# Kernel tuning notes

Hardware: AMD Instinct MI355X
Metric: run time of the kernel (lower is better)

Reference implementation:

```python
import jax, jax.numpy as jnp
import numpy as np

FIELD_DIMS = [100000, 50000, 20000, 10000, 5000, 2000, 1000, 500, 100, 26]
ORDER = 3
EMBED_DIM = 64


def setup_inputs() -> dict:
    key = jax.random.key(0)
    k1, k2, k3 = jax.random.split(key, 3)
    total = sum(FIELD_DIMS)  # 188626
    num_fields = len(FIELD_DIMS)
    batch = 16384
    x = jax.random.randint(k1, (batch, num_fields), 0, 26, dtype=jnp.int64 if jax.config.jax_enable_x64 else jnp.int32)
    offsets = jnp.asarray(np.concatenate([[0], np.cumsum(FIELD_DIMS)[:-1]]), dtype=x.dtype)
    # xavier-uniform-ish init scale for embedding table
    emb_dim_total = EMBED_DIM * (ORDER - 1)
    W_emb = jax.random.normal(k2, (total, emb_dim_total), dtype=jnp.float32) * 0.01
    W_lin = jax.random.normal(k3, (total, 1), dtype=jnp.float32) * 0.01
    bias = jnp.zeros((1,), dtype=jnp.float32)
    return {"x": x, "offsets": offsets, "W_emb": W_emb, "W_lin": W_lin, "bias": bias}


def _anova_kernel(x, order):
    # x: (B, F, D). Recursive ANOVA-kernel recurrence, Python loop over small `order`.
    B, F, D = x.shape
    a_prev = jnp.ones((B, F + 1, D), dtype=x.dtype)
    a = a_prev
    for t in range(order):
        a = jnp.zeros((B, F + 1, D), dtype=x.dtype)
        a = a.at[:, t + 1:, :].set(x[:, t:, :] * a_prev[:, t:F, :])
        a = jnp.cumsum(a, axis=1)
        a_prev = a
    return jnp.sum(a[:, -1, :], axis=-1)  # (B,)


def _fm(x):
    # x: (B, F, D) -> (B,)
    square_of_sum = jnp.sum(x, axis=1) ** 2
    sum_of_square = jnp.sum(x ** 2, axis=1)
    return 0.5 * jnp.sum(square_of_sum - sum_of_square, axis=1)


def reference(x, offsets, W_emb, W_lin, bias):
    idx = x + offsets[None, :]              # (B, F)
    # linear term: sum of per-field scalar weights + bias
    y = jnp.sum(W_lin[idx], axis=1)[:, 0] + bias[0]   # (B,)
    emb = W_emb[idx]                         # (B, F, EMBED_DIM*(ORDER-1))
    # order-2 FM on first slice
    y = y + _fm(emb[:, :, :EMBED_DIM])
    # orders 3..ORDER via ANOVA kernels on subsequent slices
    for i in range(ORDER - 2):
        x_part = emb[:, :, (i + 1) * EMBED_DIM:(i + 2) * EMBED_DIM]
        y = y + _anova_kernel(x_part, order=3 + i)
    return jax.nn.relu(y)
```

## Files before the change

kernel.cpp:

```cpp
#include <hip/hip_runtime.h>

#define NUM_FIELDS 10
#define EMB 64
#define ROW 128
#define WAVES_PER_BLOCK 4

__global__ __launch_bounds__(256) void fm_ho_kernel(
    const int* __restrict__ x, const int* __restrict__ offsets,
    const float* __restrict__ W_emb, const float* __restrict__ W_lin,
    const float* __restrict__ bias, float* __restrict__ out, int batch)
{
    const int lane = threadIdx.x & 63;
    const int wave = threadIdx.x >> 6;
    const int b = blockIdx.x * WAVES_PER_BLOCK + wave;
    if (b >= batch) return;

    int ids[NUM_FIELDS];
#pragma unroll
    for (int f = 0; f < NUM_FIELDS; ++f)
        ids[f] = x[b * NUM_FIELDS + f] + offsets[f];

    float s1a = 0.f, s2a = 0.f;
    float s1b = 0.f, s2b = 0.f, s3b = 0.f;
#pragma unroll
    for (int f = 0; f < NUM_FIELDS; ++f) {
        const float* row = W_emb + (size_t)ids[f] * ROW;
        float e1 = row[lane];
        float e2 = row[EMB + lane];
        s1a += e1;
        s2a = fmaf(e1, e1, s2a);
        s1b += e2;
        float e2sq = e2 * e2;
        s2b += e2sq;
        s3b = fmaf(e2sq, e2, s3b);
    }

    float v = 0.5f * (s1a * s1a - s2a)
            + (s1b * s1b * s1b - 3.f * s1b * s2b + 2.f * s3b) * (1.f / 6.f);

    if (lane < NUM_FIELDS) v += W_lin[ids[lane]];

#pragma unroll
    for (int off = 32; off; off >>= 1)
        v += __shfl_xor(v, off, 64);

    if (lane == 0) {
        float y = v + bias[0];
        out[b] = y > 0.f ? y : 0.f;
    }
}

extern "C" void kernel_launch(void* const* d_in, const int* in_sizes, int n_in,
                              void* d_out, int out_size, void* d_ws, size_t ws_size,
                              hipStream_t stream) {
    const int*   x       = (const int*)d_in[0];
    const int*   offsets = (const int*)d_in[1];
    const float* W_emb   = (const float*)d_in[2];
    const float* W_lin   = (const float*)d_in[3];
    const float* bias    = (const float*)d_in[4];
    float*       out     = (float*)d_out;

    const int batch = in_sizes[0] / NUM_FIELDS;
    const int grid  = (batch + WAVES_PER_BLOCK - 1) / WAVES_PER_BLOCK;
    hipLaunchKernelGGL(fm_ho_kernel, dim3(grid), dim3(256), 0, stream,
                       x, offsets, W_emb, W_lin, bias, out, batch);
}
```

Before: 132.3 us.

## Process two samples per wave with float4 row loads and half-wave reductions

```diff
diff --git a/kernel.cpp b/kernel.cpp
--- a/kernel.cpp
+++ b/kernel.cpp
@@ -1,9 +1,9 @@
 #include <hip/hip_runtime.h>
 
 #define NUM_FIELDS 10
-#define EMB 64
 #define ROW 128
 #define WAVES_PER_BLOCK 4
+#define SAMPLES_PER_BLOCK 8
 
 __global__ __launch_bounds__(256) void fm_ho_kernel(
     const int* __restrict__ x, const int* __restrict__ offsets,
@@ -12,40 +12,58 @@
 {
     const int lane = threadIdx.x & 63;
     const int wave = threadIdx.x >> 6;
-    const int b = blockIdx.x * WAVES_PER_BLOCK + wave;
+    const int half = lane >> 5;
+    const int hl   = lane & 31;
+    const int b = (blockIdx.x * WAVES_PER_BLOCK + wave) * 2 + half;
     if (b >= batch) return;
 
+    float lin = 0.f;
+    if (hl < NUM_FIELDS)
+        lin = W_lin[x[b * NUM_FIELDS + hl] + offsets[hl]];
+
     int ids[NUM_FIELDS];
+    {
+        const int2* xp = reinterpret_cast<const int2*>(x + b * NUM_FIELDS);
+        int2 p0 = xp[0], p1 = xp[1], p2 = xp[2], p3 = xp[3], p4 = xp[4];
+        ids[0] = p0.x; ids[1] = p0.y; ids[2] = p1.x; ids[3] = p1.y;
+        ids[4] = p2.x; ids[5] = p2.y; ids[6] = p3.x; ids[7] = p3.y;
+        ids[8] = p4.x; ids[9] = p4.y;
 #pragma unroll
-    for (int f = 0; f < NUM_FIELDS; ++f)
-        ids[f] = x[b * NUM_FIELDS + f] + offsets[f];
+        for (int f = 0; f < NUM_FIELDS; ++f) ids[f] += offsets[f];
+    }
 
-    float s1a = 0.f, s2a = 0.f;
-    float s1b = 0.f, s2b = 0.f, s3b = 0.f;
+    float4 s1 = make_float4(0.f, 0.f, 0.f, 0.f);
+    float4 s2 = s1, s3 = s1;
 #pragma unroll
     for (int f = 0; f < NUM_FIELDS; ++f) {
-        const float* row = W_emb + (size_t)ids[f] * ROW;
-        float e1 = row[lane];
-        float e2 = row[EMB + lane];
-        s1a += e1;
-        s2a = fmaf(e1, e1, s2a);
-        s1b += e2;
-        float e2sq = e2 * e2;
-        s2b += e2sq;
-        s3b = fmaf(e2sq, e2, s3b);
+        const float4 v = *reinterpret_cast<const float4*>(
+            W_emb + (size_t)ids[f] * ROW + 4 * hl);
+        const float tx = v.x * v.x, ty = v.y * v.y,
+                    tz = v.z * v.z, tw = v.w * v.w;
+        s1.x += v.x; s1.y += v.y; s1.z += v.z; s1.w += v.w;
+        s2.x += tx;  s2.y += ty;  s2.z += tz;  s2.w += tw;
+        s3.x = fmaf(tx, v.x, s3.x); s3.y = fmaf(ty, v.y, s3.y);
+        s3.z = fmaf(tz, v.z, s3.z); s3.w = fmaf(tw, v.w, s3.w);
     }
 
-    float v = 0.5f * (s1a * s1a - s2a)
-            + (s1b * s1b * s1b - 3.f * s1b * s2b + 2.f * s3b) * (1.f / 6.f);
-
-    if (lane < NUM_FIELDS) v += W_lin[ids[lane]];
+    float v;
+    if (hl < 16) {
+        v = 0.5f * ((s1.x * s1.x - s2.x) + (s1.y * s1.y - s2.y)
+                  + (s1.z * s1.z - s2.z) + (s1.w * s1.w - s2.w));
+    } else {
+        v = ((s1.x * (s1.x * s1.x - 3.f * s2.x) + 2.f * s3.x)
+           + (s1.y * (s1.y * s1.y - 3.f * s2.y) + 2.f * s3.y)
+           + (s1.z * (s1.z * s1.z - 3.f * s2.z) + 2.f * s3.z)
+           + (s1.w * (s1.w * s1.w - 3.f * s2.w) + 2.f * s3.w)) * (1.f / 6.f);
+    }
+    v += lin;
 
 #pragma unroll
-    for (int off = 32; off; off >>= 1)
+    for (int off = 16; off; off >>= 1)
         v += __shfl_xor(v, off, 64);
 
-    if (lane == 0) {
-        float y = v + bias[0];
+    if (hl == 0) {
+        const float y = v + bias[0];
         out[b] = y > 0.f ? y : 0.f;
     }
 }
@@ -61,7 +79,7 @@
     float*       out     = (float*)d_out;
 
     const int batch = in_sizes[0] / NUM_FIELDS;
-    const int grid  = (batch + WAVES_PER_BLOCK - 1) / WAVES_PER_BLOCK;
+    const int grid  = (batch + SAMPLES_PER_BLOCK - 1) / SAMPLES_PER_BLOCK;
     hipLaunchKernelGGL(fm_ho_kernel, dim3(grid), dim3(256), 0, stream,
                        x, offsets, W_emb, W_lin, bias, out, batch);
 }
```

New measurement: 130.6 us. Within noise of the previous version (-1.3%).
